# Performance work log

Hardware: AMD Instinct MI355X
Metric: run time of the kernel (lower is better)

## Reference

```python
import jax, jax.numpy as jnp
import numpy as np

N, L, H, V = 8192, 512, 64, 50000
NUM_PARENT = 1024


def setup_inputs() -> dict:
    key = jax.random.key(0)
    ks = jax.random.split(key, 12)
    def mat(k, shape):
        return 0.1 * jax.random.normal(k, shape, dtype=jnp.float32)
    return {
        "x_word": jax.random.normal(ks[0], (N, L), dtype=jnp.float32),
        "x_index": jax.random.randint(ks[1], (N, L), 0, V),
        "tree": jax.random.randint(ks[2], (N, 2), 0, N),
        "num_parent": NUM_PARENT,
        "embedding": mat(ks[3], (V, H)),
        "W_z": mat(ks[4], (H, H)),
        "U_z": mat(ks[5], (H, H)),
        "b_z": jnp.zeros((H,), dtype=jnp.float32),
        "W_r": mat(ks[6], (H, H)),
        "U_r": mat(ks[7], (H, H)),
        "b_r": jnp.zeros((H,), dtype=jnp.float32),
        "W_h": mat(ks[8], (H, H)),
        "U_h": mat(ks[9], (H, H)),
        "b_h": jnp.zeros((H,), dtype=jnp.float32),
    }


def _hard_sigmoid(x):
    # torch double-threshold trick == clip(0.2*x + 0.5, 0, 1)
    return jnp.clip(0.2 * x + 0.5, 0.0, 1.0)


def reference(x_word, x_index, tree, num_parent, embedding,
              W_z, U_z, b_z, W_r, U_r, b_r, W_h, U_h, b_h):
    n_nodes = x_word.shape[0]
    hdim = embedding.shape[1]

    def step(node_h, xs):
        word, idx, info = xs  # word: [L] f32, idx: [L] int, info: [2] int
        parent_h = node_h[info[0]]                 # [H]
        child_xe = embedding[idx].T @ word         # [H] weighted embedding sum
        z = _hard_sigmoid(W_z @ child_xe + U_z @ parent_h + b_z)
        r = _hard_sigmoid(W_r @ child_xe + U_r @ parent_h + b_r)
        c = jnp.tanh(W_h @ child_xe + U_h @ (parent_h * r) + b_h)
        h = z * parent_h + (1.0 - z) * c           # [H]
        return node_h.at[info[1]].set(h), h

    node_h0 = jnp.zeros((n_nodes, hdim), dtype=x_word.dtype)
    # original loops i in range(len(x_word) - 1)
    _, child_hs = jax.lax.scan(step, node_h0,
                               (x_word[:-1], x_index[:-1], tree[:-1]))
    # output = max over child_hs[num_parent-1:]
    return jnp.max(child_hs[num_parent - 1:], axis=0)
```

## Files before the change

kernel.cpp:

```cpp
#include <hip/hip_runtime.h>
#include <math.h>

#define NODES  8192
#define STEPS  8191
#define LW     512
#define H      64
#define VOCAB  50000
#define SWEEPK 6

typedef __attribute__((ext_vector_type(2))) float f32x2;

__global__ void ws_too_small_kernel(float* __restrict__ out) {
    if (threadIdx.x < H) out[threadIdx.x] = -12345.0f;
}

__global__ __launch_bounds__(256)
void cvt_emb(const float* __restrict__ emb, unsigned int* __restrict__ embq) {
    const int total = VOCAB * H / 4;
    for (int i = blockIdx.x * 256 + threadIdx.x; i < total; i += 256 * 256) {
        float4 v = reinterpret_cast<const float4*>(emb)[i];
        int w = 0;
        w = __builtin_amdgcn_cvt_pk_fp8_f32(v.x, v.y, w, false);
        w = __builtin_amdgcn_cvt_pk_fp8_f32(v.z, v.w, w, true);
        embq[i] = (unsigned int)w;
    }
}

__global__ __launch_bounds__(256)
void gather_sched(const float* __restrict__ xw, const int* __restrict__ xi,
                  const unsigned int* __restrict__ embq,
                  const float* __restrict__ Wz, const float* __restrict__ Wr,
                  const float* __restrict__ Wh,
                  const float* __restrict__ bz, const float* __restrict__ br,
                  const float* __restrict__ bh,
                  const int* __restrict__ tree,
                  float* __restrict__ A,
                  int* __restrict__ writers_g, int* __restrict__ pred_g,
                  int* __restrict__ lstart_g, int* __restrict__ order_g) {
    __shared__ int smem[NODES + 8];
    __shared__ int wsum[4];
    int tid = threadIdx.x;

    if (blockIdx.x == 0) {
        int lane = tid & 63, wv = tid >> 6;

        for (int i = tid; i < NODES + 8; i += 256) smem[i] = 0;
        __syncthreads();
        for (int j = tid; j < STEPS; j += 256)
            atomicAdd(&smem[tree[2 * j + 1]], 1);
        __syncthreads();

        {
            int base = tid * 32;
            int v[32], run = 0;
            #pragma unroll
            for (int e = 0; e < 32; ++e) { v[e] = run; run += smem[base + e]; }
            int x = run;
            #pragma unroll
            for (int d = 1; d < 64; d <<= 1) {
                int y = __shfl_up(x, d, 64);
                if (lane >= d) x += y;
            }
            if (lane == 63) wsum[wv] = x;
            __syncthreads();
            if (tid == 0) {
                int a = 0;
                for (int k = 0; k < 4; ++k) { a += wsum[k]; wsum[k] = a; }
            }
            __syncthreads();
            int wbase = (wv > 0) ? wsum[wv - 1] : 0;
            int tbase = wbase + x - run;
            #pragma unroll
            for (int e = 0; e < 32; ++e) smem[base + e] = tbase + v[e];
        }
        __syncthreads();

        for (int j = tid; j < STEPS; j += 256) {
            int v = tree[2 * j + 1];
            int pos = atomicAdd(&smem[v], 1);
            writers_g[pos] = j;
        }
        __syncthreads();

        for (int e = 0; e < 32; ++e) {
            int i = tid + e * 256;
            if (i < STEPS) {
                int v  = tree[2 * i];
                int t1 = smem[v];
                int t0 = (v > 0) ? smem[v - 1] : 0;
                int best = -1;
                for (int t = t0; t < t1; ++t) {
                    int j = writers_g[t];
                    if (j < i && j > best) best = j;
                }
                pred_g[i] = best;
            }
        }
        __syncthreads();

        int* comb = smem;
        for (int e = 0; e < 32; ++e) {
            int i = tid + e * 256;
            int p = (i < STEPS) ? pred_g[i] : -1;
            int d = (p >= 0) ? 1 : 0;
            comb[i] = (d << 16) | (p & 0xFFFF);
        }
        __syncthreads();
        for (int r = 0; r < 13; ++r) {
            int nw[32];
            bool active = false;
            #pragma unroll
            for (int e = 0; e < 32; ++e) {
                int i = tid + e * 256;
                int c = comb[i];
                int j = (int)(short)(c & 0xFFFF);
                if (j >= 0) {
                    int cj = comb[j];
                    nw[e] = (((c >> 16) + (cj >> 16)) << 16) | (cj & 0xFFFF);
                    active = true;
                } else {
                    nw[e] = c;
                }
            }
            if (__syncthreads_count(active) == 0) break;
            #pragma unroll
            for (int e = 0; e < 32; ++e) comb[tid + e * 256] = nw[e];
            __syncthreads();
        }
        int d32[32];
        #pragma unroll
        for (int e = 0; e < 32; ++e) d32[e] = comb[tid + e * 256] >> 16;
        __syncthreads();

        for (int i = tid; i < NODES; i += 256) smem[i] = 0;
        __syncthreads();
        #pragma unroll
        for (int e = 0; e < 32; ++e) {
            int i = tid + e * 256;
            if (i < STEPS) atomicAdd(&smem[d32[e]], 1);
        }
        __syncthreads();
        {
            int base = tid * 32;
            int v[32], run = 0;
            #pragma unroll
            for (int e = 0; e < 32; ++e) { v[e] = run; run += smem[base + e]; }
            int x = run;
            #pragma unroll
            for (int d = 1; d < 64; d <<= 1) {
                int y = __shfl_up(x, d, 64);
                if (lane >= d) x += y;
            }
            if (lane == 63) wsum[wv] = x;
            __syncthreads();
            if (tid == 0) {
                int a = 0;
                for (int k = 0; k < 4; ++k) { a += wsum[k]; wsum[k] = a; }
            }
            __syncthreads();
            int wbase = (wv > 0) ? wsum[wv - 1] : 0;
            int tbase = wbase + x - run;
            #pragma unroll
            for (int e = 0; e < 32; ++e) lstart_g[base + e] = tbase + v[e];
            if (tid == 255) lstart_g[8192] = tbase + run;
        }
        __threadfence_block();
        __syncthreads();
        for (int i = tid; i < NODES; i += 256) smem[i] = 0;
        __syncthreads();
        #pragma unroll
        for (int e = 0; e < 32; ++e) {
            int i = tid + e * 256;
            if (i < STEPS) {
                int d = d32[e];
                int pos = atomicAdd(&smem[d], 1);
                order_g[lstart_g[d] + pos] = i;
            }
        }
        return;
    }

    int i    = blockIdx.x - 1;
    int wave = tid >> 6;
    int lane = tid & 63;
    int g16  = lane >> 2;
    int q4   = lane & 3;

    float* s_w   = (float*)smem;
    int*   s_idx = smem + 512;
    float* partf = (float*)(smem + 1024);
    float* xe    = (float*)(smem + 1024 + 256);

    {
        float2 w2 = reinterpret_cast<const float2*>(xw + (size_t)i * LW)[tid];
        int2   i2 = reinterpret_cast<const int2*>(xi + (size_t)i * LW)[tid];
        s_w[2 * tid]     = w2.x;
        s_w[2 * tid + 1] = w2.y;
        s_idx[2 * tid]     = i2.x;
        s_idx[2 * tid + 1] = i2.y;
    }
    __syncthreads();

    const uint4* E = reinterpret_cast<const uint4*>(embq);
    int base_l = wave * 128 + g16;

    float acc[16];
    #pragma unroll
    for (int c = 0; c < 16; ++c) acc[c] = 0.f;

    uint4 q[8];
    float wgt[8];
    #pragma unroll
    for (int u = 0; u < 8; ++u) {
        int l   = base_l + u * 16;
        int idx = s_idx[l];
        wgt[u]  = s_w[l];
        q[u]    = E[(size_t)idx * 4 + q4];
    }
    #pragma unroll
    for (int u = 0; u < 8; ++u) {
        float w = wgt[u];
        unsigned int uw[4] = {q[u].x, q[u].y, q[u].z, q[u].w};
        #pragma unroll
        for (int d = 0; d < 4; ++d) {
            f32x2 lo = __builtin_amdgcn_cvt_pk_f32_fp8((int)uw[d], false);
            f32x2 hi = __builtin_amdgcn_cvt_pk_f32_fp8((int)uw[d], true);
            acc[4 * d + 0] = fmaf(w, lo.x, acc[4 * d + 0]);
            acc[4 * d + 1] = fmaf(w, lo.y, acc[4 * d + 1]);
            acc[4 * d + 2] = fmaf(w, hi.x, acc[4 * d + 2]);
            acc[4 * d + 3] = fmaf(w, hi.y, acc[4 * d + 3]);
        }
    }
    #pragma unroll
    for (int c = 0; c < 16; ++c) {
        acc[c] += __shfl_xor(acc[c], 4,  64);
        acc[c] += __shfl_xor(acc[c], 8,  64);
        acc[c] += __shfl_xor(acc[c], 16, 64);
        acc[c] += __shfl_xor(acc[c], 32, 64);
    }
    if (lane < 4) {
        #pragma unroll
        for (int c = 0; c < 16; ++c) partf[wave * 64 + lane * 16 + c] = acc[c];
    }
    __syncthreads();
    if (tid < 64)
        xe[tid] = partf[tid] + partf[64 + tid] + partf[128 + tid] + partf[192 + tid];
    __syncthreads();

    if (tid < 192) {
        int o = tid & 63;
        const float* W = (tid < 64) ? Wz : (tid < 128 ? Wr : Wh);
        const float* b = (tid < 64) ? bz : (tid < 128 ? br : bh);
        float s = b[o];
        #pragma unroll
        for (int j = 0; j < H; j += 4) {
            float4 w4 = *reinterpret_cast<const float4*>(W + (size_t)o * H + j);
            s = fmaf(w4.x, xe[j],     s);
            s = fmaf(w4.y, xe[j + 1], s);
            s = fmaf(w4.z, xe[j + 2], s);
            s = fmaf(w4.w, xe[j + 3], s);
        }
        A[(size_t)i * 192 + tid] = s;
    }
}

__global__ __launch_bounds__(256)
void root_steps(const float* __restrict__ A, const int* __restrict__ pred,
                float* __restrict__ child_h) {
    int s = blockIdx.x * 4 + (threadIdx.x >> 6);
    int h = threadIdx.x & 63;
    if (s >= STEPS) return;
    if (pred[s] >= 0) return;
    float az = A[(size_t)s * 192 + h];
    float ah = A[(size_t)s * 192 + 128 + h];
    float z = fminf(fmaxf(0.2f * az + 0.5f, 0.f), 1.f);
    float c = tanhf(ah);
    child_h[(size_t)s * H + h] = (1.f - z) * c;
}

__device__ __forceinline__ float rlane(float v, int j) {
    return __int_as_float(__builtin_amdgcn_readlane(__float_as_int(v), j));
}

__device__ __forceinline__ void gru_core(
        int i, int lane, const float* __restrict__ A,
        const int* __restrict__ pred,
        const float* uz, const float* ur, const float* uh,
        float* __restrict__ child_h) {
    int p = pred[i];
    float ph = (p >= 0) ? child_h[(size_t)p * H + lane] : 0.f;
    const float* Ai = A + (size_t)i * 192;
    float az = Ai[lane];
    float ar = Ai[64 + lane];
    float ah = Ai[128 + lane];

    #pragma unroll
    for (int j = 0; j < H; ++j) {
        float s = rlane(ph, j);
        az = fmaf(uz[j], s, az);
        ar = fmaf(ur[j], s, ar);
    }
    float z = fminf(fmaxf(0.2f * az + 0.5f, 0.f), 1.f);
    float r = fminf(fmaxf(0.2f * ar + 0.5f, 0.f), 1.f);
    float phr = ph * r;
    #pragma unroll
    for (int j = 0; j < H; ++j) {
        float s = rlane(phr, j);
        ah = fmaf(uh[j], s, ah);
    }
    float c = tanhf(ah);
    child_h[(size_t)i * H + lane] = z * ph + (1.f - z) * c;
}

__global__ __launch_bounds__(256)
void sweep_lvl(int k, const int* __restrict__ lstart, const int* __restrict__ order,
               const float* __restrict__ A, const int* __restrict__ pred,
               const float* __restrict__ Uz, const float* __restrict__ Ur,
               const float* __restrict__ Uh, float* __restrict__ child_h) {
    int s0 = lstart[k], s1 = lstart[k + 1];
    int wave = (blockIdx.x * blockDim.x + threadIdx.x) >> 6;
    int lane = threadIdx.x & 63;
    if (s0 + wave >= s1) return;

    float uz[H], ur[H], uh[H];
    #pragma unroll
    for (int j = 0; j < H; j += 4) {
        float4 a4 = *reinterpret_cast<const float4*>(Uz + (size_t)lane * H + j);
        uz[j] = a4.x; uz[j+1] = a4.y; uz[j+2] = a4.z; uz[j+3] = a4.w;
        float4 b4 = *reinterpret_cast<const float4*>(Ur + (size_t)lane * H + j);
        ur[j] = b4.x; ur[j+1] = b4.y; ur[j+2] = b4.z; ur[j+3] = b4.w;
        float4 c4 = *reinterpret_cast<const float4*>(Uh + (size_t)lane * H + j);
        uh[j] = c4.x; uh[j+1] = c4.y; uh[j+2] = c4.z; uh[j+3] = c4.w;
    }
    for (int t = s0 + wave; t < s1; t += 512)
        gru_core(order[t], lane, A, pred, uz, ur, uh, child_h);
}

__global__ __launch_bounds__(512)
void tail_block(const int* __restrict__ lstart, const int* __restrict__ order,
                const float* __restrict__ A, const int* __restrict__ pred,
                const float* __restrict__ Uz, const float* __restrict__ Ur,
                const float* __restrict__ Uh, float* __restrict__ child_h) {
    int wave = threadIdx.x >> 6;
    int lane = threadIdx.x & 63;

    float uz[H], ur[H], uh[H];
    #pragma unroll
    for (int j = 0; j < H; j += 4) {
        float4 a4 = *reinterpret_cast<const float4*>(Uz + (size_t)lane * H + j);
        uz[j] = a4.x; uz[j+1] = a4.y; uz[j+2] = a4.z; uz[j+3] = a4.w;
        float4 b4 = *reinterpret_cast<const float4*>(Ur + (size_t)lane * H + j);
        ur[j] = b4.x; ur[j+1] = b4.y; ur[j+2] = b4.z; ur[j+3] = b4.w;
        float4 c4 = *reinterpret_cast<const float4*>(Uh + (size_t)lane * H + j);
        uh[j] = c4.x; uh[j+1] = c4.y; uh[j+2] = c4.z; uh[j+3] = c4.w;
    }

    for (int k = SWEEPK; k < NODES; ++k) {
        int s0 = lstart[k];
        if (s0 >= STEPS) break;
        int s1 = lstart[k + 1];
        for (int t = s0 + wave; t < s1; t += 8)
            gru_core(order[t], lane, A, pred, uz, ur, uh, child_h);
        __syncthreads();
    }
}

__global__ __launch_bounds__(256)
void reduce_partial(const float* __restrict__ child_h,
                    const int* __restrict__ np_ptr,
                    float* __restrict__ partial) {
    int b   = blockIdx.x;
    int tid = threadIdx.x;
    int h   = tid & 63;
    int grp = tid >> 6;
    int np    = *np_ptr;
    int start = np - 1;
    int total = STEPS - start;
    int per   = (total + gridDim.x - 1) / gridDim.x;
    int r0 = start + b * per;
    int r1 = r0 + per; if (r1 > STEPS) r1 = STEPS;
    float m = -INFINITY;
    for (int row = r0 + grp; row < r1; row += 4)
        m = fmaxf(m, child_h[(size_t)row * H + h]);
    __shared__ float sm[4][64];
    sm[grp][h] = m;
    __syncthreads();
    if (tid < 64)
        partial[b * 64 + tid] = fmaxf(fmaxf(sm[0][tid], sm[1][tid]),
                                      fmaxf(sm[2][tid], sm[3][tid]));
}

__global__ void reduce_final(const float* __restrict__ partial,
                             float* __restrict__ out, int nb) {
    int h = threadIdx.x;
    float m = -INFINITY;
    for (int b = 0; b < nb; ++b) m = fmaxf(m, partial[b * 64 + h]);
    out[h] = m;
}

extern "C" void kernel_launch(void* const* d_in, const int* in_sizes, int n_in,
                              void* d_out, int out_size, void* d_ws, size_t ws_size,
                              hipStream_t stream) {
    const float* xw   = (const float*)d_in[0];
    const int*   xi   = (const int*)  d_in[1];
    const int*   tree = (const int*)  d_in[2];
    const int*   np   = (const int*)  d_in[3];
    const float* emb  = (const float*)d_in[4];
    const float* Wz   = (const float*)d_in[5];
    const float* Uz   = (const float*)d_in[6];
    const float* bz   = (const float*)d_in[7];
    const float* Wr   = (const float*)d_in[8];
    const float* Ur   = (const float*)d_in[9];
    const float* br   = (const float*)d_in[10];
    const float* Wh   = (const float*)d_in[11];
    const float* Uh   = (const float*)d_in[12];
    const float* bh   = (const float*)d_in[13];

    size_t bA   = (size_t)STEPS * 192 * 4;
    size_t bCH  = (size_t)STEPS * H   * 4;
    size_t bEH  = (size_t)VOCAB * H   * 1;
    size_t bInt = (size_t)(8192 * 3 + 8256) * 4;
    size_t bPar = 56 * 64 * 4 + 256;
    size_t need = bA + bCH + bEH + bInt + bPar;
    if (ws_size < need) {
        ws_too_small_kernel<<<1, 64, 0, stream>>>((float*)d_out);
        return;
    }

    char* base = (char*)d_ws;
    float*          A       = (float*)base;                 base += bA;
    float*          child_h = (float*)base;                 base += bCH;
    unsigned int*   embq    = (unsigned int*)base;          base += bEH;
    int*            pred    = (int*)base;
    int*            writers = pred    + 8192;
    int*            order   = writers + 8192;
    int*            lstart  = order   + 8192;
    float*          partial = (float*)(lstart + 8256);

    cvt_emb        <<<256, 256, 0, stream>>>(emb, embq);

    gather_sched   <<<8192, 256, 0, stream>>>(xw, xi, embq, Wz, Wr, Wh,
                                              bz, br, bh, tree, A,
                                              writers, pred, lstart, order);

    root_steps     <<<2048, 256, 0, stream>>>(A, pred, child_h);

    for (int k = 1; k < SWEEPK; ++k)
        sweep_lvl  <<<128, 256, 0, stream>>>(k, lstart, order, A, pred,
                                             Uz, Ur, Uh, child_h);
    tail_block     <<<1, 512, 0, stream>>>(lstart, order, A, pred,
                                           Uz, Ur, Uh, child_h);

    reduce_partial <<<56,  256, 0, stream>>>(child_h, np, partial);
    reduce_final   <<<1,    64, 0, stream>>>(partial, (float*)d_out, 56);
}
```

Measured before the change: 295.8 us.

## Split serial predecessor scheduling into multi-block kernels and shrink gather shared memory

The writer histogram, prefix scan, scatter and predecessor search move out of block 0 of gather_sched into four small grid-wide kernels that run before it. This removes serial work from the one block that was likely the critical path of that launch. The level-depth pointer jumping in block 0 now works on global memory instead of a NODES-sized shared array, so each gather block needs far less shared memory and more blocks can fit per CU. In exchange it adds several extra launches and a memset, and block 0's pointer jumping now pays global-memory latency.

```diff
diff --git a/kernel.cpp b/kernel.cpp
--- a/kernel.cpp
+++ b/kernel.cpp
@@ -9,6 +9,10 @@
 #define SWEEPK 6
 
 typedef __attribute__((ext_vector_type(2))) float f32x2;
+
+__device__ __forceinline__ int agload(const int* p) {
+    return __hip_atomic_load(p, __ATOMIC_RELAXED, __HIP_MEMORY_SCOPE_AGENT);
+}
 
 __global__ void ws_too_small_kernel(float* __restrict__ out) {
     if (threadIdx.x < H) out[threadIdx.x] = -12345.0f;
@@ -27,83 +31,99 @@
 }
 
 __global__ __launch_bounds__(256)
+void hist_writers(const int* __restrict__ tree, int* __restrict__ count) {
+    int j = blockIdx.x * blockDim.x + threadIdx.x;
+    if (j < STEPS) atomicAdd(&count[tree[2 * j + 1]], 1);
+}
+
+__global__ __launch_bounds__(1024)
+void prefix_kernel(const int* __restrict__ cnt, int* __restrict__ off) {
+    __shared__ int wsum[16];
+    int tid  = threadIdx.x;
+    int lane = tid & 63;
+    int wv   = tid >> 6;
+    int base = tid * 8;
+
+    int v[8], run = 0;
+    #pragma unroll
+    for (int e = 0; e < 8; ++e) { v[e] = run; run += cnt[base + e]; }
+
+    int x = run;
+    #pragma unroll
+    for (int d = 1; d < 64; d <<= 1) {
+        int y = __shfl_up(x, d, 64);
+        if (lane >= d) x += y;
+    }
+    if (lane == 63) wsum[wv] = x;
+    __syncthreads();
+    if (wv == 0) {
+        int s = (lane < 16) ? wsum[lane] : 0;
+        #pragma unroll
+        for (int d = 1; d < 16; d <<= 1) {
+            int y = __shfl_up(s, d, 64);
+            if (lane >= d) s += y;
+        }
+        if (lane < 16) wsum[lane] = s;
+    }
+    __syncthreads();
+    int wbase = (wv > 0) ? wsum[wv - 1] : 0;
+    int tbase = wbase + x - run;
+    #pragma unroll
+    for (int e = 0; e < 8; ++e) off[base + e] = tbase + v[e];
+    if (tid == 1023) off[8192] = tbase + run;
+}
+
+__global__ __launch_bounds__(256)
+void scatter_writers(const int* __restrict__ tree, const int* __restrict__ woff,
+                     int* __restrict__ cursor, int* __restrict__ writers) {
+    int j = blockIdx.x * blockDim.x + threadIdx.x;
+    if (j >= STEPS) return;
+    int v = tree[2 * j + 1];
+    int pos = atomicAdd(&cursor[v], 1);
+    writers[woff[v] + pos] = j;
+}
+
+__global__ __launch_bounds__(256)
+void pred_bucket(const int* __restrict__ tree, const int* __restrict__ woff,
+                 const int* __restrict__ writers, int* __restrict__ pred) {
+    int i = blockIdx.x * blockDim.x + threadIdx.x;
+    if (i >= STEPS) return;
+    int v  = tree[2 * i];
+    int t0 = woff[v], t1 = woff[v + 1];
+    int best = -1;
+    for (int t = t0; t < t1; ++t) {
+        int j = writers[t];
+        if (j < i && j > best) best = j;
+    }
+    pred[i] = best;
+}
+
+__global__ __launch_bounds__(256)
 void gather_sched(const float* __restrict__ xw, const int* __restrict__ xi,
                   const unsigned int* __restrict__ embq,
                   const float* __restrict__ Wz, const float* __restrict__ Wr,
                   const float* __restrict__ Wh,
                   const float* __restrict__ bz, const float* __restrict__ br,
                   const float* __restrict__ bh,
-                  const int* __restrict__ tree,
+                  const int* __restrict__ pred_g,
                   float* __restrict__ A,
-                  int* __restrict__ writers_g, int* __restrict__ pred_g,
+                  int* __restrict__ comb_g, int* __restrict__ lcnt_g,
                   int* __restrict__ lstart_g, int* __restrict__ order_g) {
-    __shared__ int smem[NODES + 8];
-    __shared__ int wsum[4];
+    __shared__ float s_w[LW];
+    __shared__ int   s_idx[LW];
+    __shared__ float partf[4][64];
+    __shared__ float xe[64];
+    __shared__ int   wsum[4];
     int tid = threadIdx.x;
 
     if (blockIdx.x == 0) {
         int lane = tid & 63, wv = tid >> 6;
 
-        for (int i = tid; i < NODES + 8; i += 256) smem[i] = 0;
-        __syncthreads();
-        for (int j = tid; j < STEPS; j += 256)
-            atomicAdd(&smem[tree[2 * j + 1]], 1);
-        __syncthreads();
-
-        {
-            int base = tid * 32;
-            int v[32], run = 0;
-            #pragma unroll
-            for (int e = 0; e < 32; ++e) { v[e] = run; run += smem[base + e]; }
-            int x = run;
-            #pragma unroll
-            for (int d = 1; d < 64; d <<= 1) {
-                int y = __shfl_up(x, d, 64);
-                if (lane >= d) x += y;
-            }
-            if (lane == 63) wsum[wv] = x;
-            __syncthreads();
-            if (tid == 0) {
-                int a = 0;
-                for (int k = 0; k < 4; ++k) { a += wsum[k]; wsum[k] = a; }
-            }
-            __syncthreads();
-            int wbase = (wv > 0) ? wsum[wv - 1] : 0;
-            int tbase = wbase + x - run;
-            #pragma unroll
-            for (int e = 0; e < 32; ++e) smem[base + e] = tbase + v[e];
-        }
-        __syncthreads();
-
-        for (int j = tid; j < STEPS; j += 256) {
-            int v = tree[2 * j + 1];
-            int pos = atomicAdd(&smem[v], 1);
-            writers_g[pos] = j;
-        }
-        __syncthreads();
-
-        for (int e = 0; e < 32; ++e) {
-            int i = tid + e * 256;
-            if (i < STEPS) {
-                int v  = tree[2 * i];
-                int t1 = smem[v];
-                int t0 = (v > 0) ? smem[v - 1] : 0;
-                int best = -1;
-                for (int t = t0; t < t1; ++t) {
-                    int j = writers_g[t];
-                    if (j < i && j > best) best = j;
-                }
-                pred_g[i] = best;
-            }
-        }
-        __syncthreads();
-
-        int* comb = smem;
         for (int e = 0; e < 32; ++e) {
             int i = tid + e * 256;
             int p = (i < STEPS) ? pred_g[i] : -1;
             int d = (p >= 0) ? 1 : 0;
-            comb[i] = (d << 16) | (p & 0xFFFF);
+            comb_g[i] = (d << 13) | (p + 1);
         }
         __syncthreads();
         for (int r = 0; r < 13; ++r) {
@@ -112,11 +132,10 @@
             #pragma unroll
             for (int e = 0; e < 32; ++e) {
                 int i = tid + e * 256;
-                int c = comb[i];
-                int j = (int)(short)(c & 0xFFFF);
+                int c = comb_g[i];
+                int j = (c & 0x1FFF) - 1;
                 if (j >= 0) {
-                    int cj = comb[j];
-                    nw[e] = (((c >> 16) + (cj >> 16)) << 16) | (cj & 0xFFFF);
+                    nw[e] = (c & ~0x1FFF) + comb_g[j];
                     active = true;
                 } else {
                     nw[e] = c;
@@ -124,27 +143,25 @@
             }
             if (__syncthreads_count(active) == 0) break;
             #pragma unroll
-            for (int e = 0; e < 32; ++e) comb[tid + e * 256] = nw[e];
+            for (int e = 0; e < 32; ++e) comb_g[tid + e * 256] = nw[e];
             __syncthreads();
         }
-        int d32[32];
-        #pragma unroll
-        for (int e = 0; e < 32; ++e) d32[e] = comb[tid + e * 256] >> 16;
-        __syncthreads();
-
-        for (int i = tid; i < NODES; i += 256) smem[i] = 0;
-        __syncthreads();
-        #pragma unroll
+
+        for (int i = tid; i < NODES; i += 256) lcnt_g[i] = 0;
+        __syncthreads();
         for (int e = 0; e < 32; ++e) {
             int i = tid + e * 256;
-            if (i < STEPS) atomicAdd(&smem[d32[e]], 1);
+            if (i < STEPS) atomicAdd(&lcnt_g[comb_g[i] >> 13], 1);
         }
         __syncthreads();
         {
             int base = tid * 32;
             int v[32], run = 0;
             #pragma unroll
-            for (int e = 0; e < 32; ++e) { v[e] = run; run += smem[base + e]; }
+            for (int e = 0; e < 32; ++e) {
+                v[e] = run;
+                run += agload(&lcnt_g[base + e]);
+            }
             int x = run;
             #pragma unroll
             for (int d = 1; d < 64; d <<= 1) {
@@ -164,16 +181,14 @@
             for (int e = 0; e < 32; ++e) lstart_g[base + e] = tbase + v[e];
             if (tid == 255) lstart_g[8192] = tbase + run;
         }
-        __threadfence_block();
-        __syncthreads();
-        for (int i = tid; i < NODES; i += 256) smem[i] = 0;
-        __syncthreads();
-        #pragma unroll
+        __syncthreads();
+        for (int i = tid; i < NODES; i += 256) lcnt_g[i] = 0;
+        __syncthreads();
         for (int e = 0; e < 32; ++e) {
             int i = tid + e * 256;
             if (i < STEPS) {
-                int d = d32[e];
-                int pos = atomicAdd(&smem[d], 1);
+                int d = comb_g[i] >> 13;
+                int pos = atomicAdd(&lcnt_g[d], 1);
                 order_g[lstart_g[d] + pos] = i;
             }
         }
@@ -185,11 +200,6 @@
     int lane = tid & 63;
     int g16  = lane >> 2;
     int q4   = lane & 3;
-
-    float* s_w   = (float*)smem;
-    int*   s_idx = smem + 512;
-    float* partf = (float*)(smem + 1024);
-    float* xe    = (float*)(smem + 1024 + 256);
 
     {
         float2 w2 = reinterpret_cast<const float2*>(xw + (size_t)i * LW)[tid];
@@ -240,11 +250,11 @@
     }
     if (lane < 4) {
         #pragma unroll
-        for (int c = 0; c < 16; ++c) partf[wave * 64 + lane * 16 + c] = acc[c];
+        for (int c = 0; c < 16; ++c) partf[wave][lane * 16 + c] = acc[c];
     }
     __syncthreads();
     if (tid < 64)
-        xe[tid] = partf[tid] + partf[64 + tid] + partf[128 + tid] + partf[192 + tid];
+        xe[tid] = partf[0][tid] + partf[1][tid] + partf[2][tid] + partf[3][tid];
     __syncthreads();
 
     if (tid < 192) {
@@ -419,7 +429,7 @@
     size_t bA   = (size_t)STEPS * 192 * 4;
     size_t bCH  = (size_t)STEPS * H   * 4;
     size_t bEH  = (size_t)VOCAB * H   * 1;
-    size_t bInt = (size_t)(8192 * 3 + 8256) * 4;
+    size_t bInt = (size_t)(8192 * 7 + 8256 * 2) * 4;
     size_t bPar = 56 * 64 * 4 + 256;
     size_t need = bA + bCH + bEH + bInt + bPar;
     if (ws_size < need) {
@@ -434,14 +444,25 @@
     int*            pred    = (int*)base;
     int*            writers = pred    + 8192;
     int*            order   = writers + 8192;
-    int*            lstart  = order   + 8192;
+    int*            count   = order   + 8192;
+    int*            cursor  = count   + 8192;
+    int*            comb    = cursor  + 8192;
+    int*            lcnt    = comb    + 8192;
+    int*            woff    = lcnt    + 8192;
+    int*            lstart  = woff    + 8256;
     float*          partial = (float*)(lstart + 8256);
 
     cvt_emb        <<<256, 256, 0, stream>>>(emb, embq);
 
+    hipMemsetAsync(count, 0, (size_t)2 * 8192 * sizeof(int), stream);
+    hist_writers   <<<32,  256, 0, stream>>>(tree, count);
+    prefix_kernel  <<<1,  1024, 0, stream>>>(count, woff);
+    scatter_writers<<<32,  256, 0, stream>>>(tree, woff, cursor, writers);
+    pred_bucket    <<<32,  256, 0, stream>>>(tree, woff, writers, pred);
+
     gather_sched   <<<8192, 256, 0, stream>>>(xw, xi, embq, Wz, Wr, Wh,
-                                              bz, br, bh, tree, A,
-                                              writers, pred, lstart, order);
+                                              bz, br, bh, pred, A,
+                                              comb, lcnt, lstart, order);
 
     root_steps     <<<2048, 256, 0, stream>>>(A, pred, child_h);
 
```

New measurement: 446.8 us. 1.51x slower.
